# Performance work log

Hardware: AMD Instinct MI355X
Metric: run time of the kernel (lower is better)

## Reference

```python
import jax, jax.numpy as jnp
import numpy as np

H = 16      # num_attention_heads
D = 64      # head_dim
W = 256     # one-sided attention window (tokens attend to +/- W neighbors)


def setup_inputs() -> dict:
    key = jax.random.key(0)
    ks = jax.random.split(key, 7)
    B, S, E = 2, 4096, 1024
    init = lambda k, shape: jax.random.normal(k, shape, jnp.float32) * 0.02
    return {
        "hidden_states": jax.random.normal(ks[0], (B, S, E), jnp.float32),
        "Wq": init(ks[1], (E, E)), "bq": init(ks[2], (E,)),
        "Wk": init(ks[3], (E, E)), "bk": init(ks[4], (E,)),
        "Wv": init(ks[5], (E, E)), "bv": init(ks[6], (E,)),
    }


def _sliding_window_attn(q, k, v, S):
    """q,k,v: [B,H,S,D]. Banded attention: query i attends keys |i-j|<=W.
    Implemented via overlapping chunks (sliding_chunks style), never forming SxS."""
    B = q.shape[0]
    C = S // W  # number of query chunks
    qc = q.reshape(B, H, C, W, D)

    def window(x):
        # pad one chunk each side, then stack 3 consecutive chunks per query chunk
        xp = jnp.pad(x, ((0, 0), (0, 0), (W, W), (0, 0)))
        xr = xp.reshape(B, H, C + 2, W, D)
        return jnp.concatenate([xr[:, :, i:i + C] for i in range(3)], axis=3)  # [B,H,C,3W,D]

    kc, vc = window(k), window(v)

    i = jnp.arange(W)[:, None]            # query offset within chunk
    j = jnp.arange(3 * W)[None, :]        # key offset within 3W window
    band = jnp.abs(j - W - i) <= W        # [W,3W] band mask
    kpos = jnp.arange(C)[:, None, None] * W + (j - W)[None]  # absolute key pos [C,1,3W]
    valid = band[None] & (kpos >= 0) & (kpos < S)             # [C,W,3W]

    scores = jnp.einsum('bhcqd,bhckd->bhcqk', qc, kc)         # [B,H,C,W,3W]
    scores = jnp.where(valid[None, None], scores, -jnp.inf)
    probs = jax.nn.softmax(scores, axis=-1)
    out = jnp.einsum('bhcqk,bhckd->bhcqd', probs, vc)         # [B,H,C,W,D]
    return out.reshape(B, H, S, D)


def reference(hidden_states, Wq, bq, Wk, bk, Wv, bv):
    B, S, E = hidden_states.shape
    scale = 1.0 / np.sqrt(D).astype(np.float32)

    def split_heads(x):  # [B,S,E] -> [B,H,S,D]
        return x.reshape(B, S, H, D).transpose(0, 2, 1, 3)

    q = split_heads((hidden_states @ Wq.T + bq) * scale)
    k = split_heads(hidden_states @ Wk.T + bk)
    v = split_heads(hidden_states @ Wv.T + bv)

    ctx = _sliding_window_attn(q, k, v, S)                 # [B,H,S,D]
    return ctx.transpose(0, 2, 1, 3).reshape(B, S, E)      # [B,S,E]
```

## Files before the change

### kernel.cpp

```cpp
#include <hip/hip_runtime.h>

#define NH 16
#define HD 64
#define WIN 256
#define BB 2
#define SS 4096
#define EE 1024

typedef __attribute__((ext_vector_type(8))) short short8;
typedef __attribute__((ext_vector_type(4))) float floatx4;
typedef __attribute__((ext_vector_type(4))) unsigned short ushort4v;

__device__ inline unsigned short f2bf(float f) {
    unsigned u = __builtin_bit_cast(unsigned, f);
    u += 0x7fffu + ((u >> 16) & 1u);
    return (unsigned short)(u >> 16);
}

__global__ __launch_bounds__(256)
void cvt_kernel(const float* __restrict__ X,
                const float* __restrict__ W0,
                const float* __restrict__ W1,
                const float* __restrict__ W2,
                unsigned short* __restrict__ out)
{
    size_t idx = (size_t)blockIdx.x * 256 + threadIdx.x;
    const size_t X4 = 2097152, W4 = 262144;
    const float* src; unsigned short* dst; size_t off;
    if (idx < X4)                { src = X;  dst = out;            off = idx; }
    else if (idx < X4 + W4)      { src = W0; dst = out + 8388608;  off = idx - X4; }
    else if (idx < X4 + 2 * W4)  { src = W1; dst = out + 9437184;  off = idx - X4 - W4; }
    else                         { src = W2; dst = out + 10485760; off = idx - X4 - 2 * W4; }
    float4 v = ((const float4*)src)[off];
    ushort4 u;
    u.x = f2bf(v.x); u.y = f2bf(v.y); u.z = f2bf(v.z); u.w = f2bf(v.w);
    ((ushort4*)dst)[off] = u;
}

__global__ __launch_bounds__(256, 4)
void qkv_gemm4(const unsigned short* __restrict__ Xb,
               const unsigned short* __restrict__ WbAll,
               const float* __restrict__ b0,
               const float* __restrict__ b1,
               const float* __restrict__ b2,
               unsigned short* __restrict__ Qo,
               unsigned short* __restrict__ Ko,
               unsigned short* __restrict__ Vo)
{
    const int id = blockIdx.x;
    const int xcd = id & 7;
    const int rest = id >> 3;
    const int ytile = xcd + 8 * (rest & 7);
    const int nm = rest >> 3;
    const int ntile = nm & 7;
    const int mode = nm >> 3;

    const unsigned short* Wm = WbAll + (size_t)mode * 1048576;
    const float* bm = (mode == 0) ? b0 : (mode == 1) ? b1 : b2;
    unsigned short* outp = (mode == 0) ? Qo : (mode == 1) ? Ko : Vo;

    const int m0 = ytile * 128;
    const int n0 = ntile * 128;
    const int t = threadIdx.x;
    const int lane = t & 63;
    const int wv = t >> 6;
    const int wm = wv >> 1, wn = wv & 1;
    const int lg = lane >> 4, lc = lane & 15;

    __shared__ __attribute__((aligned(16))) unsigned short smem[16384];
    unsigned short* As[2] = { smem, smem + 4096 };
    unsigned short* Bs[2] = { smem + 8192, smem + 12288 };

    const int srow = lane >> 2;
    const int scol = (lane & 3) * 8;

    floatx4 acc[4][4];
#pragma unroll
    for (int i = 0; i < 4; ++i)
#pragma unroll
        for (int j = 0; j < 4; ++j)
            acc[i][j] = (floatx4)0.0f;

    for (int kt = 0; kt < EE; kt += 64) {
        if (kt) __syncthreads();
#pragma unroll
        for (int half = 0; half < 2; ++half) {
#pragma unroll
            for (int seg = 0; seg < 2; ++seg) {
                int r0 = wv * 32 + seg * 16;
                const unsigned short* asrc =
                    Xb + (size_t)(m0 + r0 + srow) * EE + kt + half * 32 + scol;
                const unsigned short* bsrc =
                    Wm + (size_t)(n0 + r0 + srow) * EE + kt + half * 32 + scol;
                __builtin_amdgcn_global_load_lds(
                    (const __attribute__((address_space(1))) unsigned int*)asrc,
                    (__attribute__((address_space(3))) unsigned int*)&As[half][r0 * 32], 16, 0, 0);
                __builtin_amdgcn_global_load_lds(
                    (const __attribute__((address_space(1))) unsigned int*)bsrc,
                    (__attribute__((address_space(3))) unsigned int*)&Bs[half][r0 * 32], 16, 0, 0);
            }
        }
        __syncthreads();

#pragma unroll
        for (int half = 0; half < 2; ++half) {
            short8 af[4], bfr[4];
#pragma unroll
            for (int mt = 0; mt < 4; ++mt)
                af[mt] = *(const short8*)(&As[half][(wm * 64 + mt * 16 + lc) * 32 + lg * 8]);
#pragma unroll
            for (int nt = 0; nt < 4; ++nt)
                bfr[nt] = *(const short8*)(&Bs[half][(wn * 64 + nt * 16 + lc) * 32 + lg * 8]);
#pragma unroll
            for (int mt = 0; mt < 4; ++mt)
#pragma unroll
                for (int nt = 0; nt < 4; ++nt)
                    acc[mt][nt] = __builtin_amdgcn_mfma_f32_16x16x32_bf16(
                        af[mt], bfr[nt], acc[mt][nt], 0, 0, 0);
        }
    }

    const int CST = 136;
    const float qscale = (mode == 0) ? 0.125f : 1.0f;
#pragma unroll
    for (int p = 0; p < 2; ++p) {
        __syncthreads();
        if (mode < 2) {
            if (wm == p) {
#pragma unroll
                for (int nt = 0; nt < 4; ++nt) {
                    float bias = bm[n0 + wn * 64 + nt * 16 + lc];
#pragma unroll
                    for (int mt = 0; mt < 4; ++mt)
#pragma unroll
                        for (int r = 0; r < 4; ++r) {
                            int ml = mt * 16 + lg * 4 + r;
                            int nl = wn * 64 + nt * 16 + lc;
                            smem[ml * CST + nl] = f2bf((acc[mt][nt][r] + bias) * qscale);
                        }
                }
            }
        } else {
            if (wn == p) {
#pragma unroll
                for (int nt = 0; nt < 4; ++nt) {
                    float bias = bm[n0 + p * 64 + nt * 16 + lc];
#pragma unroll
                    for (int mt = 0; mt < 4; ++mt) {
                        ushort4v pk;
#pragma unroll
                        for (int r = 0; r < 4; ++r)
                            pk[r] = f2bf(acc[mt][nt][r] + bias);
                        int nl = nt * 16 + lc;
                        int col = wm * 64 + mt * 16 + lg * 4;
                        *(ushort4v*)(&smem[nl * CST + col]) = pk;
                    }
                }
            }
        }
        __syncthreads();
#pragma unroll
        for (int q = 0; q < 4; ++q) {
            int c = q * 256 + t;
            int row = c >> 4;
            int j = c & 15;
            uint4 val = *(const uint4*)(&smem[row * CST + j * 8]);
            if (mode < 2) {
                int m = m0 + p * 64 + row;
                int bb = m >> 12, s = m & (SS - 1);
                int n = n0 + j * 8;
                int hh = n >> 6, dd = n & 63;
                *(uint4*)(outp + (((size_t)bb * NH + hh) * SS + s) * HD + dd) = val;
            } else {
                int n = n0 + p * 64 + row;
                int hh = n >> 6, dd = n & 63;
                int m = m0 + j * 8;
                int bb = m >> 12, s = m & (SS - 1);
                *(uint4*)(outp + (((size_t)bb * NH + hh) * HD + dd) * SS + s) = val;
            }
        }
    }
}

__global__ __launch_bounds__(256, 2)
void swa_kernel(const unsigned short* __restrict__ Qp_,
                const unsigned short* __restrict__ Kp_,
                const unsigned short* __restrict__ Vp_,
                float* __restrict__ outp)
{
    const int h = blockIdx.x;
    const int q0 = blockIdx.y * 128;
    const int b = blockIdx.z;
    const int t = threadIdx.x, lane = t & 63, wv = t >> 6;
    const int lg = lane >> 4, lc = lane & 15;
    const size_t bh = (size_t)b * NH + h;
    const unsigned short* Qp = Qp_ + bh * (size_t)SS * HD;
    const unsigned short* Kp = Kp_ + bh * (size_t)SS * HD;
    const unsigned short* Vp = Vp_ + bh * (size_t)HD * SS;
    const int qbase = q0 + wv * 32;

    short8 qf[2][2];
#pragma unroll
    for (int rt = 0; rt < 2; ++rt)
#pragma unroll
        for (int hh = 0; hh < 2; ++hh)
            qf[rt][hh] = *(const short8*)(Qp + (size_t)(qbase + rt * 16 + lc) * HD + hh * 32 + lg * 8);

    floatx4 o[2][4];
    float lsum[2][4];
#pragma unroll
    for (int rt = 0; rt < 2; ++rt)
#pragma unroll
        for (int i = 0; i < 4; ++i) { o[rt][i] = (floatx4)0.0f; lsum[rt][i] = 0.0f; }

    __shared__ __attribute__((aligned(16))) unsigned short kvs[2][2][4096];
    __shared__ __attribute__((aligned(16))) unsigned short Ps[4][2][16][72];

    const int kbeg = (q0 >= WIN) ? (q0 - WIN) : 0;
    const int kend = (q0 + 128 + WIN <= SS) ? (q0 + 128 + WIN) : SS;

    const int sr = lane >> 3;
    const int sj = lane & 7;
    const int swz = (sj ^ sr) * 8;

#define STAGE(buf, k0_)                                                              \
    {                                                                                \
        _Pragma("unroll")                                                            \
        for (int i = 0; i < 2; ++i) {                                                \
            int rbase = 16 * wv + i * 8;                                             \
            const unsigned short* ks = Kp + (size_t)((k0_) + rbase + sr) * HD + swz; \
            const unsigned short* vs = Vp + (size_t)(rbase + sr) * SS + (k0_) + swz; \
            __builtin_amdgcn_global_load_lds(                                        \
                (const __attribute__((address_space(1))) unsigned int*)ks,           \
                (__attribute__((address_space(3))) unsigned int*)&kvs[buf][0][rbase * 64], 16, 0, 0); \
            __builtin_amdgcn_global_load_lds(                                        \
                (const __attribute__((address_space(1))) unsigned int*)vs,           \
                (__attribute__((address_space(3))) unsigned int*)&kvs[buf][1][rbase * 64], 16, 0, 0); \
        }                                                                            \
    }

    STAGE(0, kbeg)

    int cur = 0;
    for (int k0 = kbeg; k0 < kend; k0 += 64, cur ^= 1) {
        __syncthreads();
        bool active = (k0 + 63 >= qbase - WIN) && (k0 <= qbase + 31 + WIN);
        short8 kc[4][2], vf[4][2];
        if (active) {
#pragma unroll
            for (int nt = 0; nt < 4; ++nt)
#pragma unroll
                for (int hh = 0; hh < 2; ++hh) {
                    int row = nt * 16 + lc;
                    kc[nt][hh] = *(const short8*)(&kvs[cur][0][row * 64 + (((hh * 4 + lg) ^ (row & 7)) * 8)]);
                    vf[nt][hh] = *(const short8*)(&kvs[cur][1][row * 64 + (((hh * 4 + lg) ^ (row & 7)) * 8)]);
                }
        }
        if (k0 + 64 < kend) STAGE(cur ^ 1, k0 + 64)
        if (!active) continue;

        bool fullband = (k0 >= qbase - 225) && (k0 <= qbase + 193);

        floatx4 sc[2][4];
#pragma unroll
        for (int rt = 0; rt < 2; ++rt)
#pragma unroll
            for (int nt = 0; nt < 4; ++nt) {
                floatx4 z = (floatx4)0.0f;
                z = __builtin_amdgcn_mfma_f32_16x16x32_bf16(qf[rt][0], kc[nt][0], z, 0, 0, 0);
                sc[rt][nt] = __builtin_amdgcn_mfma_f32_16x16x32_bf16(qf[rt][1], kc[nt][1], z, 0, 0, 0);
            }
#pragma unroll
        for (int rt = 0; rt < 2; ++rt)
#pragma unroll
            for (int nt = 0; nt < 4; ++nt)
#pragma unroll
                for (int r = 0; r < 4; ++r)
                    sc[rt][nt][r] = __expf(sc[rt][nt][r]);
        if (!fullband) {
#pragma unroll
            for (int rt = 0; rt < 2; ++rt)
#pragma unroll
                for (int nt = 0; nt < 4; ++nt) {
                    int kk = k0 + nt * 16 + lc;
#pragma unroll
                    for (int r = 0; r < 4; ++r) {
                        int dq = (qbase + rt * 16 + lg * 4 + r) - kk;
                        if (dq > WIN || dq < -WIN) sc[rt][nt][r] = 0.0f;
                    }
                }
        }
#pragma unroll
        for (int rt = 0; rt < 2; ++rt)
#pragma unroll
            for (int r = 0; r < 4; ++r)
                lsum[rt][r] += (sc[rt][0][r] + sc[rt][1][r]) + (sc[rt][2][r] + sc[rt][3][r]);
#pragma unroll
        for (int rt = 0; rt < 2; ++rt)
#pragma unroll
            for (int nt = 0; nt < 4; ++nt)
#pragma unroll
                for (int r = 0; r < 4; ++r)
                    Ps[wv][rt][lg * 4 + r][nt * 16 + lc] = f2bf(sc[rt][nt][r]);
#pragma unroll
        for (int rt = 0; rt < 2; ++rt) {
            short8 pa0 = *(const short8*)(&Ps[wv][rt][lc][lg * 8]);
            short8 pa1 = *(const short8*)(&Ps[wv][rt][lc][32 + lg * 8]);
#pragma unroll
            for (int nt2 = 0; nt2 < 4; ++nt2) {
                o[rt][nt2] = __builtin_amdgcn_mfma_f32_16x16x32_bf16(pa0, vf[nt2][0], o[rt][nt2], 0, 0, 0);
                o[rt][nt2] = __builtin_amdgcn_mfma_f32_16x16x32_bf16(pa1, vf[nt2][1], o[rt][nt2], 0, 0, 0);
            }
        }
    }

#pragma unroll
    for (int rt = 0; rt < 2; ++rt)
#pragma unroll
        for (int r = 0; r < 4; ++r) {
            float rs = lsum[rt][r];
#pragma unroll
            for (int off = 1; off < 16; off <<= 1)
                rs += __shfl_xor(rs, off, 64);
            lsum[rt][r] = 1.0f / rs;
        }
#pragma unroll
    for (int rt = 0; rt < 2; ++rt)
#pragma unroll
        for (int nt2 = 0; nt2 < 4; ++nt2)
#pragma unroll
            for (int r = 0; r < 4; ++r) {
                int q = qbase + rt * 16 + lg * 4 + r;
                int d = nt2 * 16 + lc;
                outp[((size_t)b * SS + q) * EE + h * HD + d] = o[rt][nt2][r] * lsum[rt][r];
            }
}

extern "C" void kernel_launch(void* const* d_in, const int* in_sizes, int n_in,
                              void* d_out, int out_size, void* d_ws, size_t ws_size,
                              hipStream_t stream) {
    const float* X  = (const float*)d_in[0];
    const float* Wq = (const float*)d_in[1];
    const float* bq = (const float*)d_in[2];
    const float* Wk = (const float*)d_in[3];
    const float* bk = (const float*)d_in[4];
    const float* Wv = (const float*)d_in[5];
    const float* bv = (const float*)d_in[6];

    const size_t qkv_elems = (size_t)BB * NH * SS * HD;
    unsigned short* Qw = (unsigned short*)d_ws;
    unsigned short* Kw = Qw + qkv_elems;
    unsigned short* Vw = Kw + qkv_elems;

    unsigned short* cvt = (unsigned short*)d_out;
    const unsigned short* Xb = cvt;
    const unsigned short* WbAll = cvt + 8388608;

    cvt_kernel<<<dim3(11264), 256, 0, stream>>>(X, Wq, Wk, Wv, cvt);
    qkv_gemm4<<<dim3(1536), 256, 0, stream>>>(
        Xb, WbAll, bq, bk, bv, Qw, Kw, Vw);
    swa_kernel<<<dim3(NH, SS / 128, BB), 256, 0, stream>>>(Qw, Kw, Vw, (float*)d_out);
}
```

Measured before the change: 194.8 us.

## Rewrite QKV GEMM as 256x256 8-wave tile with ping-pong LDS pipeline

Replaces the 128x128, 4-wave QKV projection GEMM with a 256x256 tile computed by 8 waves. It uses a double-buffered 128KB LDS with XOR-swizzled layout, interleaves global-to-LDS staging with quarter-tile MFMA phases behind explicit barriers and vmcnt waits, and raises MFMA priority with setprio. Block ordering is swizzled so tiles group per XCD. The aims are more data reuse per loaded byte, fewer LDS bank conflicts and overlap of loads with compute. The cost is far fewer blocks (384), heavy LDS use that limits occupancy to one block per CU, and a fragile hand-written sync schedule.

Measured after the change: 204.1 us. 1.05x slower.

```diff
diff --git a/kernel.cpp b/kernel.cpp
--- a/kernel.cpp
+++ b/kernel.cpp
@@ -37,8 +37,8 @@
     ((ushort4*)dst)[off] = u;
 }
 
-__global__ __launch_bounds__(256, 4)
-void qkv_gemm4(const unsigned short* __restrict__ Xb,
+__global__ __launch_bounds__(512, 2)
+void qkv_gemm8(const unsigned short* __restrict__ Xb,
                const unsigned short* __restrict__ WbAll,
                const float* __restrict__ b0,
                const float* __restrict__ b1,
@@ -48,81 +48,142 @@
                unsigned short* __restrict__ Vo)
 {
     const int id = blockIdx.x;
-    const int xcd = id & 7;
-    const int rest = id >> 3;
-    const int ytile = xcd + 8 * (rest & 7);
-    const int nm = rest >> 3;
-    const int ntile = nm & 7;
-    const int mode = nm >> 3;
+    const int swz = (id & 7) * 48 + (id >> 3);
+    const int mtile = swz / 12;
+    const int rem = swz - mtile * 12;
+    const int mode = rem >> 2;
+    const int ntile = rem & 3;
 
     const unsigned short* Wm = WbAll + (size_t)mode * 1048576;
     const float* bm = (mode == 0) ? b0 : (mode == 1) ? b1 : b2;
     unsigned short* outp = (mode == 0) ? Qo : (mode == 1) ? Ko : Vo;
-
-    const int m0 = ytile * 128;
-    const int n0 = ntile * 128;
+    const int m0 = mtile * 256;
+    const int n0 = ntile * 256;
+
     const int t = threadIdx.x;
     const int lane = t & 63;
-    const int wv = t >> 6;
-    const int wm = wv >> 1, wn = wv & 1;
+    const int w = t >> 6;
+    const int wm = w >> 2;
+    const int wn = w & 3;
     const int lg = lane >> 4, lc = lane & 15;
 
-    __shared__ __attribute__((aligned(16))) unsigned short smem[16384];
-    unsigned short* As[2] = { smem, smem + 4096 };
-    unsigned short* Bs[2] = { smem + 8192, smem + 12288 };
-
-    const int srow = lane >> 2;
-    const int scol = (lane & 3) * 8;
-
-    floatx4 acc[4][4];
-#pragma unroll
-    for (int i = 0; i < 4; ++i)
+    __shared__ __attribute__((aligned(16))) unsigned short smem[65536];
+
+#define STAGE8(ab, half, ktile)                                                        \
+    {                                                                                  \
+        unsigned short* bse_ = smem + ((((ktile) & 1) * 2 + (ab)) * 2 + (half)) * 8192;\
+        _Pragma("unroll")                                                              \
+        for (int i_ = 0; i_ < 2; ++i_) {                                               \
+            const int rl_ = (i_ * 8 + w) * 8 + (lane >> 3);                            \
+            const int cs_ = (lane & 7) ^ (lane >> 3);                                  \
+            const unsigned short* src_ = ((ab) ? Wm : Xb) +                            \
+                (size_t)(((ab) ? n0 : m0) + (half) * 128 + rl_) * EE +                 \
+                (ktile) * 64 + cs_ * 8;                                                \
+            __builtin_amdgcn_global_load_lds(                                          \
+                (const __attribute__((address_space(1))) unsigned int*)src_,           \
+                (__attribute__((address_space(3))) unsigned int*)(bse_ + (i_ * 8 + w) * 512), \
+                16, 0, 0);                                                             \
+        }                                                                              \
+    }
+
+    const int swk0 = ((0 + lg) ^ (lc & 7)) * 8;
+    const int swk1 = ((4 + lg) ^ (lc & 7)) * 8;
+
+#define LDA8(buf, mq, m, kh) \
+    (*(const short8*)(smem + ((buf) * 4 + wm) * 8192 + ((mq) * 64 + (m) * 16 + lc) * 64 + ((kh) ? swk1 : swk0)))
+#define LDB8(buf, nq, nn, kh) \
+    (*(const short8*)(smem + ((buf) * 4 + 2 + (wn >> 1)) * 8192 + ((wn & 1) * 4096 + ((nq) * 32 + (nn) * 16 + lc) * 64) + ((kh) ? swk1 : swk0)))
+
+#define RDA(buf, mq)                                         \
+    _Pragma("unroll")                                        \
+    for (int m_ = 0; m_ < 4; ++m_) {                         \
+        af[m_][0] = LDA8(buf, mq, m_, 0);                    \
+        af[m_][1] = LDA8(buf, mq, m_, 1);                    \
+    }
+#define RDB(buf, nq)                                         \
+    _Pragma("unroll")                                        \
+    for (int n_ = 0; n_ < 2; ++n_) {                         \
+        bf[(nq) * 2 + n_][0] = LDB8(buf, nq, n_, 0);         \
+        bf[(nq) * 2 + n_][1] = LDB8(buf, nq, n_, 1);         \
+    }
+
+#define MFMAQ(MQ, NQ)                                                               \
+    __builtin_amdgcn_s_setprio(1);                                                  \
+    _Pragma("unroll")                                                               \
+    for (int m_ = 0; m_ < 4; ++m_) {                                                \
+        _Pragma("unroll")                                                           \
+        for (int n_ = 0; n_ < 2; ++n_) {                                            \
+            acc[(MQ) * 4 + m_][(NQ) * 2 + n_] = __builtin_amdgcn_mfma_f32_16x16x32_bf16( \
+                af[m_][0], bf[(NQ) * 2 + n_][0], acc[(MQ) * 4 + m_][(NQ) * 2 + n_], 0, 0, 0); \
+            acc[(MQ) * 4 + m_][(NQ) * 2 + n_] = __builtin_amdgcn_mfma_f32_16x16x32_bf16( \
+                af[m_][1], bf[(NQ) * 2 + n_][1], acc[(MQ) * 4 + m_][(NQ) * 2 + n_], 0, 0, 0); \
+        }                                                                           \
+    }                                                                               \
+    __builtin_amdgcn_s_setprio(0);
+
+    floatx4 acc[8][4];
+#pragma unroll
+    for (int i = 0; i < 8; ++i)
 #pragma unroll
         for (int j = 0; j < 4; ++j)
             acc[i][j] = (floatx4)0.0f;
 
-    for (int kt = 0; kt < EE; kt += 64) {
-        if (kt) __syncthreads();
-#pragma unroll
-        for (int half = 0; half < 2; ++half) {
-#pragma unroll
-            for (int seg = 0; seg < 2; ++seg) {
-                int r0 = wv * 32 + seg * 16;
-                const unsigned short* asrc =
-                    Xb + (size_t)(m0 + r0 + srow) * EE + kt + half * 32 + scol;
-                const unsigned short* bsrc =
-                    Wm + (size_t)(n0 + r0 + srow) * EE + kt + half * 32 + scol;
-                __builtin_amdgcn_global_load_lds(
-                    (const __attribute__((address_space(1))) unsigned int*)asrc,
-                    (__attribute__((address_space(3))) unsigned int*)&As[half][r0 * 32], 16, 0, 0);
-                __builtin_amdgcn_global_load_lds(
-                    (const __attribute__((address_space(1))) unsigned int*)bsrc,
-                    (__attribute__((address_space(3))) unsigned int*)&Bs[half][r0 * 32], 16, 0, 0);
-            }
-        }
-        __syncthreads();
-
-#pragma unroll
-        for (int half = 0; half < 2; ++half) {
-            short8 af[4], bfr[4];
-#pragma unroll
-            for (int mt = 0; mt < 4; ++mt)
-                af[mt] = *(const short8*)(&As[half][(wm * 64 + mt * 16 + lc) * 32 + lg * 8]);
-#pragma unroll
-            for (int nt = 0; nt < 4; ++nt)
-                bfr[nt] = *(const short8*)(&Bs[half][(wn * 64 + nt * 16 + lc) * 32 + lg * 8]);
-#pragma unroll
-            for (int mt = 0; mt < 4; ++mt)
-#pragma unroll
-                for (int nt = 0; nt < 4; ++nt)
-                    acc[mt][nt] = __builtin_amdgcn_mfma_f32_16x16x32_bf16(
-                        af[mt], bfr[nt], acc[mt][nt], 0, 0, 0);
-        }
-    }
-
-    const int CST = 136;
+    short8 af[4][2], bf[4][2];
+
+    STAGE8(1, 0, 0) STAGE8(0, 0, 0) STAGE8(1, 1, 0) STAGE8(0, 1, 0)
+    STAGE8(1, 0, 1) STAGE8(0, 0, 1)
+    asm volatile("s_waitcnt vmcnt(4)" ::: "memory");
+    __builtin_amdgcn_s_barrier();
+
+#pragma unroll 1
+    for (int J = 0; J < 8; ++J) {
+        const int kb = 2 * J;
+        RDA(0, 0) RDB(0, 0)
+        STAGE8(1, 1, kb + 1)
+        __builtin_amdgcn_s_barrier();
+        MFMAQ(0, 0)
+        __builtin_amdgcn_s_barrier();
+        RDB(0, 1)
+        STAGE8(0, 1, kb + 1)
+        __builtin_amdgcn_s_barrier();
+        MFMAQ(0, 1)
+        __builtin_amdgcn_s_barrier();
+        RDA(0, 1)
+        if (J < 7) STAGE8(1, 0, kb + 2)
+        __builtin_amdgcn_s_barrier();
+        MFMAQ(1, 1)
+        __builtin_amdgcn_s_barrier();
+        if (J < 7) STAGE8(0, 0, kb + 2)
+        __builtin_amdgcn_s_barrier();
+        MFMAQ(1, 0)
+        if (J < 7) { asm volatile("s_waitcnt vmcnt(4)" ::: "memory"); }
+        else       { asm volatile("s_waitcnt vmcnt(0)" ::: "memory"); }
+        __builtin_amdgcn_s_barrier();
+        RDA(1, 0) RDB(1, 0)
+        if (J < 7) STAGE8(1, 1, kb + 2)
+        __builtin_amdgcn_s_barrier();
+        MFMAQ(0, 0)
+        __builtin_amdgcn_s_barrier();
+        RDB(1, 1)
+        if (J < 7) STAGE8(0, 1, kb + 2)
+        __builtin_amdgcn_s_barrier();
+        MFMAQ(0, 1)
+        __builtin_amdgcn_s_barrier();
+        RDA(1, 1)
+        if (J < 7) STAGE8(1, 0, kb + 3)
+        __builtin_amdgcn_s_barrier();
+        MFMAQ(1, 1)
+        __builtin_amdgcn_s_barrier();
+        if (J < 7) STAGE8(0, 0, kb + 3)
+        __builtin_amdgcn_s_barrier();
+        MFMAQ(1, 0)
+        if (J < 7) { asm volatile("s_waitcnt vmcnt(4)" ::: "memory"); }
+        __builtin_amdgcn_s_barrier();
+    }
+
     const float qscale = (mode == 0) ? 0.125f : 1.0f;
-#pragma unroll
+    const int CST = 264;
+#pragma unroll 1
     for (int p = 0; p < 2; ++p) {
         __syncthreads();
         if (mode < 2) {
@@ -131,55 +192,61 @@
                 for (int nt = 0; nt < 4; ++nt) {
                     float bias = bm[n0 + wn * 64 + nt * 16 + lc];
 #pragma unroll
-                    for (int mt = 0; mt < 4; ++mt)
+                    for (int mt = 0; mt < 8; ++mt)
 #pragma unroll
                         for (int r = 0; r < 4; ++r) {
-                            int ml = mt * 16 + lg * 4 + r;
-                            int nl = wn * 64 + nt * 16 + lc;
-                            smem[ml * CST + nl] = f2bf((acc[mt][nt][r] + bias) * qscale);
+                            int row = mt * 16 + lg * 4 + r;
+                            int col = wn * 64 + nt * 16 + lc;
+                            smem[row * CST + col] = f2bf((acc[mt][nt][r] + bias) * qscale);
                         }
                 }
             }
         } else {
-            if (wn == p) {
+            if ((wn >> 1) == p) {
 #pragma unroll
                 for (int nt = 0; nt < 4; ++nt) {
-                    float bias = bm[n0 + p * 64 + nt * 16 + lc];
-#pragma unroll
-                    for (int mt = 0; mt < 4; ++mt) {
+                    float bias = bm[n0 + wn * 64 + nt * 16 + lc];
+#pragma unroll
+                    for (int mt = 0; mt < 8; ++mt) {
                         ushort4v pk;
 #pragma unroll
                         for (int r = 0; r < 4; ++r)
                             pk[r] = f2bf(acc[mt][nt][r] + bias);
-                        int nl = nt * 16 + lc;
-                        int col = wm * 64 + mt * 16 + lg * 4;
-                        *(ushort4v*)(&smem[nl * CST + col]) = pk;
+                        int coll = (wn & 1) * 64 + nt * 16 + lc;
+                        int mrow = wm * 128 + mt * 16 + lg * 4;
+                        *(ushort4v*)(&smem[coll * CST + mrow]) = pk;
                     }
                 }
             }
         }
         __syncthreads();
 #pragma unroll
-        for (int q = 0; q < 4; ++q) {
-            int c = q * 256 + t;
-            int row = c >> 4;
-            int j = c & 15;
+        for (int q = 0; q < 8; ++q) {
+            int c = q * 512 + t;
+            int row = c >> 5;
+            int j = c & 31;
             uint4 val = *(const uint4*)(&smem[row * CST + j * 8]);
             if (mode < 2) {
-                int m = m0 + p * 64 + row;
-                int bb = m >> 12, s = m & (SS - 1);
+                int m = m0 + p * 128 + row;
+                int bb_ = m >> 12, s = m & (SS - 1);
                 int n = n0 + j * 8;
                 int hh = n >> 6, dd = n & 63;
-                *(uint4*)(outp + (((size_t)bb * NH + hh) * SS + s) * HD + dd) = val;
+                *(uint4*)(outp + (((size_t)bb_ * NH + hh) * SS + s) * HD + dd) = val;
             } else {
-                int n = n0 + p * 64 + row;
+                int n = n0 + p * 128 + row;
                 int hh = n >> 6, dd = n & 63;
                 int m = m0 + j * 8;
-                int bb = m >> 12, s = m & (SS - 1);
-                *(uint4*)(outp + (((size_t)bb * NH + hh) * HD + dd) * SS + s) = val;
-            }
-        }
-    }
+                int bb_ = m >> 12, s = m & (SS - 1);
+                *(uint4*)(outp + (((size_t)bb_ * NH + hh) * HD + dd) * SS + s) = val;
+            }
+        }
+    }
+#undef STAGE8
+#undef LDA8
+#undef LDB8
+#undef RDA
+#undef RDB
+#undef MFMAQ
 }
 
 __global__ __launch_bounds__(256, 2)
@@ -357,7 +424,7 @@
     const unsigned short* WbAll = cvt + 8388608;
 
     cvt_kernel<<<dim3(11264), 256, 0, stream>>>(X, Wq, Wk, Wv, cvt);
-    qkv_gemm4<<<dim3(1536), 256, 0, stream>>>(
+    qkv_gemm8<<<dim3(384), 512, 0, stream>>>(
         Xb, WbAll, bq, bk, bv, Qw, Kw, Vw);
     swa_kernel<<<dim3(NH, SS / 128, BB), 256, 0, stream>>>(Qw, Kw, Vw, (float*)d_out);
 }
```

## Enlarge QKV GEMM tile to 256x128 with 512-thread blocks

Applied to the files above, without the earlier changes.

Doubles the M dimension of the QKV projection tile to 256 rows using eight waves per block, so each weight tile loaded into LDS is reused across twice as many activation rows. Grid halves to 768 blocks and LDS grows to 48KB, and the epilogue staging is restructured for the larger tile. This reduces global/L2 traffic for the weight operand but lowers block count and may reduce occupancy.

Measured after the change: 430.5 us. +121.0%, slower.

```diff
diff --git a/kernel.cpp b/kernel.cpp
--- a/kernel.cpp
+++ b/kernel.cpp
@@ -37,7 +37,7 @@
     ((ushort4*)dst)[off] = u;
 }
 
-__global__ __launch_bounds__(256, 4)
+__global__ __launch_bounds__(512, 6)
 void qkv_gemm4(const unsigned short* __restrict__ Xb,
                const unsigned short* __restrict__ WbAll,
                const float* __restrict__ b0,
@@ -50,8 +50,8 @@
     const int id = blockIdx.x;
     const int xcd = id & 7;
     const int rest = id >> 3;
-    const int ytile = xcd + 8 * (rest & 7);
-    const int nm = rest >> 3;
+    const int mtile = xcd + 8 * (rest & 3);
+    const int nm = rest >> 2;
     const int ntile = nm & 7;
     const int mode = nm >> 3;
 
@@ -59,17 +59,18 @@
     const float* bm = (mode == 0) ? b0 : (mode == 1) ? b1 : b2;
     unsigned short* outp = (mode == 0) ? Qo : (mode == 1) ? Ko : Vo;
 
-    const int m0 = ytile * 128;
+    const int m0 = mtile * 256;
     const int n0 = ntile * 128;
     const int t = threadIdx.x;
     const int lane = t & 63;
     const int wv = t >> 6;
-    const int wm = wv >> 1, wn = wv & 1;
+    const int wm = wv >> 1;
+    const int wn = wv & 1;
     const int lg = lane >> 4, lc = lane & 15;
 
-    __shared__ __attribute__((aligned(16))) unsigned short smem[16384];
-    unsigned short* As[2] = { smem, smem + 4096 };
-    unsigned short* Bs[2] = { smem + 8192, smem + 12288 };
+    __shared__ __attribute__((aligned(16))) unsigned short smem[24576];
+    unsigned short* As[2] = { smem, smem + 8192 };
+    unsigned short* Bs[2] = { smem + 16384, smem + 20480 };
 
     const int srow = lane >> 2;
     const int scol = (lane & 3) * 8;
@@ -90,14 +91,17 @@
                 int r0 = wv * 32 + seg * 16;
                 const unsigned short* asrc =
                     Xb + (size_t)(m0 + r0 + srow) * EE + kt + half * 32 + scol;
-                const unsigned short* bsrc =
-                    Wm + (size_t)(n0 + r0 + srow) * EE + kt + half * 32 + scol;
                 __builtin_amdgcn_global_load_lds(
                     (const __attribute__((address_space(1))) unsigned int*)asrc,
                     (__attribute__((address_space(3))) unsigned int*)&As[half][r0 * 32], 16, 0, 0);
+            }
+            {
+                int rb = wv * 16;
+                const unsigned short* bsrc =
+                    Wm + (size_t)(n0 + rb + srow) * EE + kt + half * 32 + scol;
                 __builtin_amdgcn_global_load_lds(
                     (const __attribute__((address_space(1))) unsigned int*)bsrc,
-                    (__attribute__((address_space(3))) unsigned int*)&Bs[half][r0 * 32], 16, 0, 0);
+                    (__attribute__((address_space(3))) unsigned int*)&Bs[half][rb * 32], 16, 0, 0);
             }
         }
         __syncthreads();
@@ -120,13 +124,13 @@
         }
     }
 
-    const int CST = 136;
     const float qscale = (mode == 0) ? 0.125f : 1.0f;
 #pragma unroll
     for (int p = 0; p < 2; ++p) {
         __syncthreads();
         if (mode < 2) {
-            if (wm == p) {
+            const int CST = 136;
+            if ((wm >> 1) == p) {
 #pragma unroll
                 for (int nt = 0; nt < 4; ++nt) {
                     float bias = bm[n0 + wn * 64 + nt * 16 + lc];
@@ -134,13 +138,27 @@
                     for (int mt = 0; mt < 4; ++mt)
 #pragma unroll
                         for (int r = 0; r < 4; ++r) {
-                            int ml = mt * 16 + lg * 4 + r;
+                            int ml = (wm & 1) * 64 + mt * 16 + lg * 4 + r;
                             int nl = wn * 64 + nt * 16 + lc;
                             smem[ml * CST + nl] = f2bf((acc[mt][nt][r] + bias) * qscale);
                         }
                 }
             }
+            __syncthreads();
+#pragma unroll
+            for (int q = 0; q < 4; ++q) {
+                int c = q * 512 + t;
+                int row = c >> 4;
+                int j = c & 15;
+                uint4 val = *(const uint4*)(&smem[row * CST + j * 8]);
+                int m = m0 + p * 128 + row;
+                int bb = m >> 12, s = m & (SS - 1);
+                int n = n0 + j * 8;
+                int hh = n >> 6, dd = n & 63;
+                *(uint4*)(outp + (((size_t)bb * NH + hh) * SS + s) * HD + dd) = val;
+            }
         } else {
+            const int CSTm = 264;
             if (wn == p) {
 #pragma unroll
                 for (int nt = 0; nt < 4; ++nt) {
@@ -153,25 +171,17 @@
                             pk[r] = f2bf(acc[mt][nt][r] + bias);
                         int nl = nt * 16 + lc;
                         int col = wm * 64 + mt * 16 + lg * 4;
-                        *(ushort4v*)(&smem[nl * CST + col]) = pk;
+                        *(ushort4v*)(&smem[nl * CSTm + col]) = pk;
                     }
                 }
             }
-        }
-        __syncthreads();
-#pragma unroll
-        for (int q = 0; q < 4; ++q) {
-            int c = q * 256 + t;
-            int row = c >> 4;
-            int j = c & 15;
-            uint4 val = *(const uint4*)(&smem[row * CST + j * 8]);
-            if (mode < 2) {
-                int m = m0 + p * 64 + row;
-                int bb = m >> 12, s = m & (SS - 1);
-                int n = n0 + j * 8;
-                int hh = n >> 6, dd = n & 63;
-                *(uint4*)(outp + (((size_t)bb * NH + hh) * SS + s) * HD + dd) = val;
-            } else {
+            __syncthreads();
+#pragma unroll
+            for (int q = 0; q < 4; ++q) {
+                int c = q * 512 + t;
+                int row = c >> 5;
+                int j = c & 31;
+                uint4 val = *(const uint4*)(&smem[row * CSTm + j * 8]);
                 int n = n0 + p * 64 + row;
                 int hh = n >> 6, dd = n & 63;
                 int m = m0 + j * 8;
@@ -357,7 +367,7 @@
     const unsigned short* WbAll = cvt + 8388608;
 
     cvt_kernel<<<dim3(11264), 256, 0, stream>>>(X, Wq, Wk, Wv, cvt);
-    qkv_gemm4<<<dim3(1536), 256, 0, stream>>>(
+    qkv_gemm4<<<dim3(768), 512, 0, stream>>>(
         Xb, WbAll, bq, bk, bv, Qw, Kw, Vw);
     swa_kernel<<<dim3(NH, SS / 128, BB), 256, 0, stream>>>(Qw, Kw, Vw, (float*)d_out);
 }
```
